# Kernel tuning notes

Hardware: AMD Instinct MI355X
Metric: run time of the kernel (lower is better)

## Reference

```python
import jax, jax.numpy as jnp
import numpy as np

# ClusterBlock passes CGAT(f0, f1, t, v, ...): CGAT's alpha positional gets v=325,
# so the LeakyReLU negative slope inside CGAT is 325.0 (faithful to source).
SLOPE = 325.0
NEG_INF = -9.0e15


def _leaky(x):
    return jnp.where(x >= 0, x, SLOPE * x)


def _cgat_stack(x, adj, W, Wb, Wt, a, offset):
    """Batched CGAT over (num_graph, k) sub-layers for one atrous offset.
    x: (b,v,t,f0); adj: (G,v,v) int; W:(G,K,f1,f0); Wb:(G,K,f1); Wt:(G,K,t); a:(G,K,2*f1).
    Returns (G,K,b,v,t,f1)."""
    b = x.shape[0]
    f1 = W.shape[-2]
    # h = leaky(W x + b): (G,K,b,v,t,f1)
    h = _leaky(jnp.einsum('bvtc,gkfc->gkbvtf', x, W) + Wb[:, :, None, None, None, :])
    # ht = mean over batch of Wt applied along t (no bias): (G,K,v,f1)
    ht = jnp.einsum('gkbvtf,gkt->gkvf', h, Wt) / b
    a1, a2 = a[..., :f1], a[..., f1:]          # attention vector halves
    ht_s = ht[:, :, offset::2]                  # sampled nodes (G,K,va,f1)
    # e[i,j] = leaky(a1.ht[sampled_j] + a2.ht[i]): (G,K,v,va)
    e = _leaky(jnp.einsum('gkjf,gkf->gkj', ht_s, a1)[:, :, None, :]
               + jnp.einsum('gkif,gkf->gki', ht, a2)[:, :, :, None])
    mask = (adj[:, None, :, offset::2] > 0)     # (G,1,v,va)
    att = jax.nn.softmax(jnp.where(mask, e, NEG_INF), axis=-1)
    # h_prime[b,i] = sum_j att[i,j] * h[b, sampled_j]
    hp = jnp.einsum('gkbjtf,gkij->gkbitf', h[:, :, :, offset::2], att)
    return _leaky(hp)


def setup_inputs() -> dict:
    key = jax.random.key(0)
    ks = jax.random.split(key, 8)
    B, V, T, F0, F1, K, G = 16, 325, 12, 64, 64, 4, 3
    x = jax.random.normal(ks[0], (B, V, T, F0), dtype=jnp.float32)
    graphs = jax.random.randint(ks[1], (G, V, V), 0, 2, dtype=jnp.int32)
    # params: axis 2 indexes the two atrous offsets (GC_layers1 / GC_layers2)
    W = jax.random.normal(ks[2], (G, K, 2, F1, F0), dtype=jnp.float32) * 0.02
    Wb = jax.random.normal(ks[3], (G, K, 2, F1), dtype=jnp.float32) * 0.02
    Wt = jax.random.normal(ks[4], (G, K, 2, T), dtype=jnp.float32) * 0.1
    a = jax.random.normal(ks[5], (G, K, 2, 2 * F1), dtype=jnp.float32) * 0.1
    cluster_W = jax.random.normal(ks[6], (G, K, T * F0), dtype=jnp.float32) * 0.02
    return {"x": x, "graphs": graphs, "W": W, "Wb": Wb, "Wt": Wt, "a": a,
            "cluster_W": cluster_W}


def reference(x, graphs, W, Wb, Wt, a, cluster_W):
    b, v, t, f0 = x.shape
    G = cluster_W.shape[0]
    xv = x.reshape(b, v, t * f0)
    # per-graph soft cluster assignments: (G,b,v,k)
    cluster = jax.nn.softmax(jnp.einsum('bvd,gkd->gbvk', xv, cluster_W), axis=-1)
    # gc1 (offset 0) + gc2 (offset 1): (G,K,b,v,t,f1)
    gc = (_cgat_stack(x, graphs, W[:, :, 0], Wb[:, :, 0], Wt[:, :, 0], a[:, :, 0], 0)
          + _cgat_stack(x, graphs, W[:, :, 1], Wb[:, :, 1], Wt[:, :, 1], a[:, :, 1], 1))
    # weight by cluster prob, sum over k, mean over graphs
    gc_act = jnp.einsum('gkbvtf,gbvk->bvtf', gc, cluster) / G
    return gc_act, cluster
```

## Files before the change

kernel.cpp:

```cpp
#include <hip/hip_runtime.h>
#include <math.h>

namespace {

typedef __attribute__((ext_vector_type(8))) short bf16x8;
typedef __attribute__((ext_vector_type(4))) float f32x4;

constexpr int B = 16, V = 325, T = 12, F = 64, K = 4, G = 3;
constexpr int D = T * F;
constexpr int ATT_R = 336;
constexpr int ATT_S = 192;
constexpr int OUT0 = B * V * T * F;
constexpr int HT_SZ = G * K * 2 * V * F;
constexpr float SLOPE_ = 325.0f;
constexpr float NEGINF = -9.0e15f;

__device__ __forceinline__ float leaky(float x) { return x >= 0.0f ? x : SLOPE_ * x; }

__device__ __forceinline__ unsigned short f2bf(float f) {
  unsigned int u = __float_as_uint(f);
  u = (u + 0x7fffu + ((u >> 16) & 1u)) >> 16;
  return (unsigned short)u;
}
__device__ __forceinline__ float bf2f(unsigned short h) {
  return __uint_as_float((unsigned int)h << 16);
}

__device__ __forceinline__ float wsum(float v) {
#pragma unroll
  for (int m = 32; m >= 1; m >>= 1) v += __shfl_xor(v, m);
  return v;
}
__device__ __forceinline__ float wmax(float v) {
#pragma unroll
  for (int m = 32; m >= 1; m >>= 1) v = fmaxf(v, __shfl_xor(v, m));
  return v;
}

__global__ __launch_bounds__(256) void k_cluster(const float* __restrict__ x,
                                                 const float* __restrict__ cw,
                                                 float* __restrict__ out) {
  const int bv = blockIdx.x;
  const int lane = threadIdx.x & 63, wave = threadIdx.x >> 6;
  __shared__ float lg[12];
  const float* xr = x + bv * D;
  for (int p = wave; p < 12; p += 4) {
    const float* wr = cw + p * D;
    float s = 0.f;
#pragma unroll
    for (int m = 0; m < 12; ++m) {
      const int d = lane + 64 * m;
      s = fmaf(xr[d], wr[d], s);
    }
    s = wsum(s);
    if (lane == 0) lg[p] = s;
  }
  __syncthreads();
  if (threadIdx.x < 3) {
    const int g = threadIdx.x;
    float m = lg[g * 4];
    for (int k = 1; k < 4; ++k) m = fmaxf(m, lg[g * 4 + k]);
    float e[4], s = 0.f;
    for (int k = 0; k < 4; ++k) { e[k] = expf(lg[g * 4 + k] - m); s += e[k]; }
    const float inv = 1.f / s;
    const int b = bv / V, v = bv % V;
    float* o = out + OUT0 + ((g * B + b) * V + v) * K;
    for (int k = 0; k < 4; ++k) o[k] = e[k] * inv;
  }
}

__global__ __launch_bounds__(512, 4) void k_ht(const float* __restrict__ x,
                                               const float* __restrict__ W,
                                               const float* __restrict__ Wbias,
                                               const float* __restrict__ Wt,
                                               float* __restrict__ ht) {
  const int v = blockIdx.x;
  const int tid = threadIdx.x;
  const int lane = tid & 63;
  const int wv = tid >> 6;
  const int lr = lane & 15, lg = lane >> 4;
  const int n = wv & 3, half = wv >> 2;

  __shared__ unsigned short Xhi[192 * 64];
  __shared__ unsigned short Xlo[192 * 64];
  __shared__ unsigned short Whi[64 * 64];
  __shared__ unsigned short Wlo[64 * 64];
  __shared__ float biasl[64];
  __shared__ float Wtl[12];
  __shared__ float red[4][2][16];

  for (int idx = tid; idx < 192 * 8; idx += 512) {
    const int row = idx >> 3, c0 = (idx & 7) * 8;
    const int bb = row / 12, tt = row % 12;
    const float* xp = x + ((bb * V + v) * T + tt) * F + c0;
    const float4 x0 = *(const float4*)xp;
    const float4 x1 = *(const float4*)(xp + 4);
    const float vals[8] = {x0.x, x0.y, x0.z, x0.w, x1.x, x1.y, x1.z, x1.w};
    union { unsigned short u[8]; uint4 q; } H, L;
#pragma unroll
    for (int e = 0; e < 8; ++e) {
      const unsigned short hh = f2bf(vals[e]);
      H.u[e] = hh;
      L.u[e] = f2bf(vals[e] - bf2f(hh));
    }
    const int off = (row * 128 + c0 * 2) ^ ((row & 7) << 4);
    *(uint4*)((char*)Xhi + off) = H.q;
    *(uint4*)((char*)Xlo + off) = L.q;
  }

  for (int gko = 0; gko < 24; ++gko) {
    {
      const int f = tid >> 3, c0 = (tid & 7) * 8;
      const float* wp = W + gko * (F * F) + f * 64 + c0;
      const float4 w0 = *(const float4*)wp;
      const float4 w1 = *(const float4*)(wp + 4);
      const float vals[8] = {w0.x, w0.y, w0.z, w0.w, w1.x, w1.y, w1.z, w1.w};
      union { unsigned short u[8]; uint4 q; } H, L;
#pragma unroll
      for (int e = 0; e < 8; ++e) {
        const unsigned short hh = f2bf(vals[e]);
        H.u[e] = hh;
        L.u[e] = f2bf(vals[e] - bf2f(hh));
      }
      const int off = (f * 128 + c0 * 2) ^ ((f & 7) << 4);
      *(uint4*)((char*)Whi + off) = H.q;
      *(uint4*)((char*)Wlo + off) = L.q;
      if (tid < 64) biasl[tid] = Wbias[gko * 64 + tid];
      else if (tid < 76) Wtl[tid - 64] = Wt[gko * 12 + (tid - 64)];
    }
    __syncthreads();

    float psum = 0.f;
    const float bv = biasl[n * 16 + lr];
    const int offB0 = ((n * 16 + lr) * 128) ^ (((n * 16 + lr) & 7) << 4);
#pragma unroll
    for (int i = 0; i < 6; ++i) {
      const int mt = half * 6 + i;
      const int arow = mt * 16 + lr;
      const int offA0 = (arow * 128) ^ ((arow & 7) << 4);
      f32x4 acc = (f32x4){0.f, 0.f, 0.f, 0.f};
#pragma unroll
      for (int kst = 0; kst < 2; ++kst) {
        const int kb = (kst * 32 + lg * 8) * 2;
        const bf16x8 ah = *(const bf16x8*)((const char*)Xhi + (offA0 ^ kb));
        const bf16x8 al = *(const bf16x8*)((const char*)Xlo + (offA0 ^ kb));
        const bf16x8 bh = *(const bf16x8*)((const char*)Whi + (offB0 ^ kb));
        const bf16x8 bl = *(const bf16x8*)((const char*)Wlo + (offB0 ^ kb));
        acc = __builtin_amdgcn_mfma_f32_16x16x32_bf16(ah, bh, acc, 0, 0, 0);
        acc = __builtin_amdgcn_mfma_f32_16x16x32_bf16(ah, bl, acc, 0, 0, 0);
        acc = __builtin_amdgcn_mfma_f32_16x16x32_bf16(al, bh, acc, 0, 0, 0);
      }
#pragma unroll
      for (int r = 0; r < 4; ++r) {
        const int row = mt * 16 + lg * 4 + r;
        psum = fmaf(leaky(acc[r] + bv), Wtl[row % 12], psum);
      }
    }
    psum += __shfl_xor(psum, 16);
    psum += __shfl_xor(psum, 32);
    if (lg == 0) red[n][half][lr] = psum;
    __syncthreads();
    if (tid < 64)
      ht[(gko * V + v) * 64 + tid] =
          (red[tid >> 4][0][tid & 15] + red[tid >> 4][1][tid & 15]) * (1.0f / 16.0f);
    __syncthreads();
  }
}

__global__ __launch_bounds__(256) void k_att(const float* __restrict__ ht,
                                             const float* __restrict__ a,
                                             const int* __restrict__ adj,
                                             unsigned short* __restrict__ att) {
  const int gko = blockIdx.x;
  const int o = gko & 1;
  const int g = gko >> 3;
  const int Vs = o ? 162 : 163;
  const int tid = threadIdx.x, lane = tid & 63, wave = tid >> 6;
  __shared__ float s1[163], s2[325];
  const float* htg = ht + gko * (V * F);
  const float* a1 = a + gko * 128;
  const float* a2 = a1 + 64;

  for (int d = wave; d < 325 + Vs; d += 4) {
    int row; const float* av;
    if (d < 325) { row = d;                 av = a2; }
    else         { row = o + 2 * (d - 325); av = a1; }
    float s = htg[row * 64 + lane] * av[lane];
    s = wsum(s);
    if (lane == 0) { if (d < 325) s2[d] = s; else s1[d - 325] = s; }
  }
  __syncthreads();

  const int* adjg = adj + g * (V * V);
  for (int i = wave; i < V; i += 4) {
    const float e0 = s2[i];
    float vj[3];
    float mx = NEGINF;
#pragma unroll
    for (int r = 0; r < 3; ++r) {
      const int j = lane + 64 * r;
      float val = NEGINF;
      if (j < Vs) {
        const float e = leaky(s1[j] + e0);
        const int ad = adjg[i * V + (o + 2 * j)];
        val = (ad > 0) ? e : NEGINF;
      }
      vj[r] = val;
      mx = fmaxf(mx, val);
    }
    mx = wmax(mx);
    float sum = 0.f, ex[3];
#pragma unroll
    for (int r = 0; r < 3; ++r) {
      const int j = lane + 64 * r;
      const float tt = (j < Vs) ? expf(vj[r] - mx) : 0.f;
      ex[r] = tt; sum += tt;
    }
    sum = wsum(sum);
    const float inv = 1.f / sum;
    unsigned short* ar = att + ((size_t)gko * ATT_R + i) * ATT_S;
#pragma unroll
    for (int r = 0; r < 3; ++r) {
      const int j = lane + 64 * r;
      ar[j] = (j < Vs) ? f2bf(ex[r] * inv) : 0;
    }
  }
  unsigned short* zb = att + ((size_t)gko * ATT_R + 325) * ATT_S;
  for (int idx = tid; idx < (ATT_R - V) * ATT_S; idx += 256) zb[idx] = 0;
}

__global__ __launch_bounds__(512, 2) void k_hp(const float* __restrict__ x,
                                               const float* __restrict__ W,
                                               const float* __restrict__ Wbias,
                                               const unsigned short* __restrict__ att,
                                               const float* __restrict__ cluster,
                                               float* __restrict__ out) {
  const int bid = blockIdx.x;
  const int o = bid & 1;
  const int g = (bid >> 1) % 3;
  const int bt = bid / 6;
  const int t = bt % 12;
  const int b = bt / 12;
  const int Vs = o ? 162 : 163;
  const int tid = threadIdx.x;
  const int lane = tid & 63;
  const int wv = tid >> 6;
  const int lr = lane & 15;
  const int lg = lane >> 4;

  __shared__ unsigned short Xl[176 * 64];
  __shared__ unsigned short Wlb[64 * 64];
  __shared__ unsigned short Htl[64 * 192];
  __shared__ float biasl[64];
  __shared__ float cll[336 * 4];

  for (int idx = tid; idx < 176 * 8; idx += 512) {
    const int j = idx >> 3, c0 = (idx & 7) * 8;
    union { unsigned short u[8]; uint4 q; } P;
    if (j < Vs) {
      const float* xp = x + ((b * V + (o + 2 * j)) * T + t) * F + c0;
      const float4 x0 = *(const float4*)xp;
      const float4 x1 = *(const float4*)(xp + 4);
      P.u[0] = f2bf(x0.x); P.u[1] = f2bf(x0.y); P.u[2] = f2bf(x0.z); P.u[3] = f2bf(x0.w);
      P.u[4] = f2bf(x1.x); P.u[5] = f2bf(x1.y); P.u[6] = f2bf(x1.z); P.u[7] = f2bf(x1.w);
    } else {
      P.q = make_uint4(0, 0, 0, 0);
    }
    *(uint4*)((char*)Xl + ((j * 128 + c0 * 2) ^ ((j & 7) << 4))) = P.q;
  }
  for (int i = tid; i < 336; i += 512) {
    float4 c4 = make_float4(0.f, 0.f, 0.f, 0.f);
    if (i < V) c4 = *(const float4*)(cluster + ((g * B + b) * V + i) * K);
    *(float4*)&cll[i * 4] = c4;
  }
  for (int idx = tid; idx < (64 * 192) / 8; idx += 512)
    ((uint4*)Htl)[idx] = make_uint4(0, 0, 0, 0);

  f32x4 accO[3][4];
#pragma unroll
  for (int s = 0; s < 3; ++s)
#pragma unroll
    for (int n = 0; n < 4; ++n) accO[s][n] = (f32x4){0.f, 0.f, 0.f, 0.f};

  for (int k = 0; k < K; ++k) {
    const int gko = (g * K + k) * 2 + o;
    __syncthreads();
    {
      const int f = tid >> 3, c0 = (tid & 7) * 8;
      const float* wp = W + gko * (F * F) + f * 64 + c0;
      const float4 w0 = *(const float4*)wp;
      const float4 w1 = *(const float4*)(wp + 4);
      union { unsigned short u[8]; uint4 q; } P;
      P.u[0] = f2bf(w0.x); P.u[1] = f2bf(w0.y); P.u[2] = f2bf(w0.z); P.u[3] = f2bf(w0.w);
      P.u[4] = f2bf(w1.x); P.u[5] = f2bf(w1.y); P.u[6] = f2bf(w1.z); P.u[7] = f2bf(w1.w);
      *(uint4*)((char*)Wlb + ((f * 128 + c0 * 2) ^ ((f & 7) << 4))) = P.q;
      if (tid < 64) biasl[tid] = Wbias[gko * 64 + tid];
    }
    __syncthreads();

    for (int s = 0; s < 6; ++s) {
      const int p = wv + 8 * s;
      if (p < 44) {
        const int mt = p >> 2, n = p & 3;
        f32x4 acc = (f32x4){0.f, 0.f, 0.f, 0.f};
#pragma unroll
        for (int kst = 0; kst < 2; ++kst) {
          const int j = mt * 16 + lr, k0 = kst * 32 + lg * 8;
          const bf16x8 af = *(const bf16x8*)((const char*)Xl + ((j * 128 + k0 * 2) ^ ((j & 7) << 4)));
          const int f = n * 16 + lr;
          const bf16x8 bf = *(const bf16x8*)((const char*)Wlb + ((f * 128 + k0 * 2) ^ ((f & 7) << 4)));
          acc = __builtin_amdgcn_mfma_f32_16x16x32_bf16(af, bf, acc, 0, 0, 0);
        }
        const int f = n * 16 + lr;
        const float bv = biasl[f];
        const int j0 = mt * 16 + lg * 4;
        union { unsigned short u[4]; uint2 q; } Pk;
#pragma unroll
        for (int r = 0; r < 4; ++r) {
          const float val = leaky(acc[r] + bv);
          Pk.u[r] = (j0 + r < Vs) ? f2bf(val) : 0;
        }
        *(uint2*)((char*)Htl + ((f * 384 + j0 * 2) ^ ((f & 7) << 4))) = Pk.q;
      }
    }
    __syncthreads();

    f32x4 accC[3][4];
#pragma unroll
    for (int s = 0; s < 3; ++s)
#pragma unroll
      for (int n = 0; n < 4; ++n) accC[s][n] = (f32x4){0.f, 0.f, 0.f, 0.f};

    const unsigned short* ab = att + (size_t)gko * (ATT_R * ATT_S);
#pragma unroll 2
    for (int kst = 0; kst < 6; ++kst) {
      const int kk0 = kst * 32 + lg * 8;
      bf16x8 bfr[4];
#pragma unroll
      for (int n = 0; n < 4; ++n) {
        const int f = n * 16 + lr;
        bfr[n] = *(const bf16x8*)((const char*)Htl + ((f * 384 + kk0 * 2) ^ ((f & 7) << 4)));
      }
#pragma unroll
      for (int s = 0; s < 3; ++s) {
        const int mt = wv + 8 * s;
        if (mt < 21) {
          const bf16x8 af = *(const bf16x8*)(ab + (mt * 16 + lr) * ATT_S + kk0);
#pragma unroll
          for (int n = 0; n < 4; ++n)
            accC[s][n] = __builtin_amdgcn_mfma_f32_16x16x32_bf16(af, bfr[n], accC[s][n], 0, 0, 0);
        }
      }
    }
#pragma unroll
    for (int s = 0; s < 3; ++s) {
      const int mt = wv + 8 * s;
      if (mt < 21) {
        const int i0 = mt * 16 + lg * 4;
#pragma unroll
        for (int r = 0; r < 4; ++r) {
          const float clv = cll[(i0 + r) * 4 + k];
#pragma unroll
          for (int n = 0; n < 4; ++n)
            accO[s][n][r] += leaky(accC[s][n][r]) * clv;
        }
      }
    }
  }

#pragma unroll
  for (int s = 0; s < 3; ++s) {
    const int mt = wv + 8 * s;
    if (mt < 21) {
      const int i0 = mt * 16 + lg * 4;
#pragma unroll
      for (int r = 0; r < 4; ++r) {
        const int i = i0 + r;
        if (i < V) {
          float* op = out + ((b * V + i) * T + t) * F + lr;
#pragma unroll
          for (int n = 0; n < 4; ++n)
            atomicAdd(op + n * 16, accO[s][n][r] * (1.0f / 3.0f));
        }
      }
    }
  }
}

}

extern "C" void kernel_launch(void* const* d_in, const int* in_sizes, int n_in,
                              void* d_out, int out_size, void* d_ws, size_t ws_size,
                              hipStream_t stream) {
  const float* x   = (const float*)d_in[0];
  const int*   adj = (const int*)d_in[1];
  const float* W   = (const float*)d_in[2];
  const float* Wb  = (const float*)d_in[3];
  const float* Wt  = (const float*)d_in[4];
  const float* a   = (const float*)d_in[5];
  const float* cw  = (const float*)d_in[6];
  float* out = (float*)d_out;
  float* ws  = (float*)d_ws;

  float* ht = ws;
  unsigned short* attw = (unsigned short*)(ws + HT_SZ);

  hipMemsetAsync(out, 0, (size_t)OUT0 * sizeof(float), stream);
  k_cluster<<<B * V, 256, 0, stream>>>(x, cw, out);
  k_ht<<<V, 512, 0, stream>>>(x, W, Wb, Wt, ht);
  k_att<<<G * K * 2, 256, 0, stream>>>(ht, a, adj, attw);
  k_hp<<<B * T * G * 2, 512, 0, stream>>>(x, W, Wb, attw, out + OUT0, out);
}
```

Measured before the change: 397.3 us.

## Replace output atomics with partial buffers plus reduction kernel; keep W fragments in registers

k_hp now writes each (graph, offset) block's weighted result to a separate partial buffer in workspace, and a new k_red kernel sums the six partials and scales by 1/3. This replaces the float atomicAdd epilogue and the output memset, provided the workspace is large enough; otherwise it falls back to the atomic path. W fragments and bias are loaded straight into registers and prefetched for the next k, which removes the shared W tile and one barrier per k. It also zeroes only the padding part of Htl, raises launch bounds to 4 blocks per SM, and fully unrolls the attention loop. The cost is roughly 100MB of extra partial-buffer traffic and higher register pressure.

```diff
diff --git a/kernel.cpp b/kernel.cpp
--- a/kernel.cpp
+++ b/kernel.cpp
@@ -14,6 +14,12 @@
 constexpr int HT_SZ = G * K * 2 * V * F;
 constexpr float SLOPE_ = 325.0f;
 constexpr float NEGINF = -9.0e15f;
+
+constexpr size_t HT_BYTES   = (size_t)HT_SZ * 4;
+constexpr size_t ATT_BYTES  = (size_t)24 * ATT_R * ATT_S * 2;
+constexpr size_t PART_OFF_B = HT_BYTES + ATT_BYTES;
+constexpr size_t PART_BYTES = (size_t)6 * 192 * 336 * 64 * 4;
+constexpr size_t WS_NEED    = PART_OFF_B + PART_BYTES;
 
 __device__ __forceinline__ float leaky(float x) { return x >= 0.0f ? x : SLOPE_ * x; }
 
@@ -229,12 +235,13 @@
   for (int idx = tid; idx < (ATT_R - V) * ATT_S; idx += 256) zb[idx] = 0;
 }
 
-__global__ __launch_bounds__(512, 2) void k_hp(const float* __restrict__ x,
+__global__ __launch_bounds__(512, 4) void k_hp(const float* __restrict__ x,
                                                const float* __restrict__ W,
                                                const float* __restrict__ Wbias,
                                                const unsigned short* __restrict__ att,
                                                const float* __restrict__ cluster,
-                                               float* __restrict__ out) {
+                                               float* __restrict__ out,
+                                               float* __restrict__ part) {
   const int bid = blockIdx.x;
   const int o = bid & 1;
   const int g = (bid >> 1) % 3;
@@ -247,11 +254,11 @@
   const int wv = tid >> 6;
   const int lr = lane & 15;
   const int lg = lane >> 4;
+  const int n = wv & 3;
+  const int halfw = wv >> 2;
 
   __shared__ unsigned short Xl[176 * 64];
-  __shared__ unsigned short Wlb[64 * 64];
   __shared__ unsigned short Htl[64 * 192];
-  __shared__ float biasl[64];
   __shared__ float cll[336 * 4];
 
   for (int idx = tid; idx < 176 * 8; idx += 512) {
@@ -273,55 +280,78 @@
     if (i < V) c4 = *(const float4*)(cluster + ((g * B + b) * V + i) * K);
     *(float4*)&cll[i * 4] = c4;
   }
-  for (int idx = tid; idx < (64 * 192) / 8; idx += 512)
-    ((uint4*)Htl)[idx] = make_uint4(0, 0, 0, 0);
+  if (tid < 128) {
+    const int f = tid >> 1, j0 = 176 + (tid & 1) * 8;
+    *(uint4*)((char*)Htl + ((f * 384 + j0 * 2) ^ ((f & 7) << 4))) = make_uint4(0, 0, 0, 0);
+  }
+
+  const int f_row = n * 16 + lr;
+  float4 praw[2][2];
+  float bias_now;
+  {
+    const int gko0 = (g * K + 0) * 2 + o;
+    const float* wp = W + gko0 * (F * F) + f_row * 64 + lg * 8;
+#pragma unroll
+    for (int kst = 0; kst < 2; ++kst) {
+      praw[kst][0] = *(const float4*)(wp + kst * 32);
+      praw[kst][1] = *(const float4*)(wp + kst * 32 + 4);
+    }
+    bias_now = Wbias[gko0 * 64 + f_row];
+  }
 
   f32x4 accO[3][4];
 #pragma unroll
   for (int s = 0; s < 3; ++s)
 #pragma unroll
-    for (int n = 0; n < 4; ++n) accO[s][n] = (f32x4){0.f, 0.f, 0.f, 0.f};
+    for (int nn = 0; nn < 4; ++nn) accO[s][nn] = (f32x4){0.f, 0.f, 0.f, 0.f};
 
   for (int k = 0; k < K; ++k) {
     const int gko = (g * K + k) * 2 + o;
     __syncthreads();
-    {
-      const int f = tid >> 3, c0 = (tid & 7) * 8;
-      const float* wp = W + gko * (F * F) + f * 64 + c0;
-      const float4 w0 = *(const float4*)wp;
-      const float4 w1 = *(const float4*)(wp + 4);
-      union { unsigned short u[8]; uint4 q; } P;
-      P.u[0] = f2bf(w0.x); P.u[1] = f2bf(w0.y); P.u[2] = f2bf(w0.z); P.u[3] = f2bf(w0.w);
-      P.u[4] = f2bf(w1.x); P.u[5] = f2bf(w1.y); P.u[6] = f2bf(w1.z); P.u[7] = f2bf(w1.w);
-      *(uint4*)((char*)Wlb + ((f * 128 + c0 * 2) ^ ((f & 7) << 4))) = P.q;
-      if (tid < 64) biasl[tid] = Wbias[gko * 64 + tid];
-    }
-    __syncthreads();
-
+
+    bf16x8 wf[2];
+#pragma unroll
+    for (int kst = 0; kst < 2; ++kst) {
+      const float vals[8] = {praw[kst][0].x, praw[kst][0].y, praw[kst][0].z, praw[kst][0].w,
+                             praw[kst][1].x, praw[kst][1].y, praw[kst][1].z, praw[kst][1].w};
+      union { unsigned short u[8]; bf16x8 v; } P;
+#pragma unroll
+      for (int e = 0; e < 8; ++e) P.u[e] = f2bf(vals[e]);
+      wf[kst] = P.v;
+    }
+    const float bnow = bias_now;
+
+#pragma unroll
     for (int s = 0; s < 6; ++s) {
-      const int p = wv + 8 * s;
-      if (p < 44) {
-        const int mt = p >> 2, n = p & 3;
+      const int mt = halfw + 2 * s;
+      if (mt < 11) {
         f32x4 acc = (f32x4){0.f, 0.f, 0.f, 0.f};
 #pragma unroll
         for (int kst = 0; kst < 2; ++kst) {
           const int j = mt * 16 + lr, k0 = kst * 32 + lg * 8;
           const bf16x8 af = *(const bf16x8*)((const char*)Xl + ((j * 128 + k0 * 2) ^ ((j & 7) << 4)));
-          const int f = n * 16 + lr;
-          const bf16x8 bf = *(const bf16x8*)((const char*)Wlb + ((f * 128 + k0 * 2) ^ ((f & 7) << 4)));
-          acc = __builtin_amdgcn_mfma_f32_16x16x32_bf16(af, bf, acc, 0, 0, 0);
-        }
-        const int f = n * 16 + lr;
-        const float bv = biasl[f];
+          acc = __builtin_amdgcn_mfma_f32_16x16x32_bf16(af, wf[kst], acc, 0, 0, 0);
+        }
         const int j0 = mt * 16 + lg * 4;
         union { unsigned short u[4]; uint2 q; } Pk;
 #pragma unroll
         for (int r = 0; r < 4; ++r) {
-          const float val = leaky(acc[r] + bv);
+          const float val = leaky(acc[r] + bnow);
           Pk.u[r] = (j0 + r < Vs) ? f2bf(val) : 0;
         }
-        *(uint2*)((char*)Htl + ((f * 384 + j0 * 2) ^ ((f & 7) << 4))) = Pk.q;
-      }
+        *(uint2*)((char*)Htl + ((f_row * 384 + j0 * 2) ^ ((f_row & 7) << 4))) = Pk.q;
+      }
+    }
+
+    if (k < 3) {
+      const int gkon = (g * K + (k + 1)) * 2 + o;
+      const float* wp = W + gkon * (F * F) + f_row * 64 + lg * 8;
+#pragma unroll
+      for (int kst = 0; kst < 2; ++kst) {
+        praw[kst][0] = *(const float4*)(wp + kst * 32);
+        praw[kst][1] = *(const float4*)(wp + kst * 32 + 4);
+      }
+      bias_now = Wbias[gkon * 64 + f_row];
     }
     __syncthreads();
 
@@ -329,17 +359,17 @@
 #pragma unroll
     for (int s = 0; s < 3; ++s)
 #pragma unroll
-      for (int n = 0; n < 4; ++n) accC[s][n] = (f32x4){0.f, 0.f, 0.f, 0.f};
+      for (int nn = 0; nn < 4; ++nn) accC[s][nn] = (f32x4){0.f, 0.f, 0.f, 0.f};
 
     const unsigned short* ab = att + (size_t)gko * (ATT_R * ATT_S);
-#pragma unroll 2
+#pragma unroll
     for (int kst = 0; kst < 6; ++kst) {
       const int kk0 = kst * 32 + lg * 8;
       bf16x8 bfr[4];
 #pragma unroll
-      for (int n = 0; n < 4; ++n) {
-        const int f = n * 16 + lr;
-        bfr[n] = *(const bf16x8*)((const char*)Htl + ((f * 384 + kk0 * 2) ^ ((f & 7) << 4)));
+      for (int nn = 0; nn < 4; ++nn) {
+        const int f = nn * 16 + lr;
+        bfr[nn] = *(const bf16x8*)((const char*)Htl + ((f * 384 + kk0 * 2) ^ ((f & 7) << 4)));
       }
 #pragma unroll
       for (int s = 0; s < 3; ++s) {
@@ -347,8 +377,8 @@
         if (mt < 21) {
           const bf16x8 af = *(const bf16x8*)(ab + (mt * 16 + lr) * ATT_S + kk0);
 #pragma unroll
-          for (int n = 0; n < 4; ++n)
-            accC[s][n] = __builtin_amdgcn_mfma_f32_16x16x32_bf16(af, bfr[n], accC[s][n], 0, 0, 0);
+          for (int nn = 0; nn < 4; ++nn)
+            accC[s][nn] = __builtin_amdgcn_mfma_f32_16x16x32_bf16(af, bfr[nn], accC[s][nn], 0, 0, 0);
         }
       }
     }
@@ -361,30 +391,69 @@
         for (int r = 0; r < 4; ++r) {
           const float clv = cll[(i0 + r) * 4 + k];
 #pragma unroll
-          for (int n = 0; n < 4; ++n)
-            accO[s][n][r] += leaky(accC[s][n][r]) * clv;
-        }
-      }
-    }
-  }
-
-#pragma unroll
-  for (int s = 0; s < 3; ++s) {
-    const int mt = wv + 8 * s;
-    if (mt < 21) {
-      const int i0 = mt * 16 + lg * 4;
-#pragma unroll
-      for (int r = 0; r < 4; ++r) {
-        const int i = i0 + r;
-        if (i < V) {
-          float* op = out + ((b * V + i) * T + t) * F + lr;
-#pragma unroll
-          for (int n = 0; n < 4; ++n)
-            atomicAdd(op + n * 16, accO[s][n][r] * (1.0f / 3.0f));
-        }
-      }
-    }
-  }
+          for (int nn = 0; nn < 4; ++nn)
+            accO[s][nn][r] += leaky(accC[s][nn][r]) * clv;
+        }
+      }
+    }
+  }
+
+  if (part) {
+    float* pb = part + (((size_t)(g * 2 + o) * 192 + bt) * 336) * 64;
+#pragma unroll
+    for (int s = 0; s < 3; ++s) {
+      const int mt = wv + 8 * s;
+      if (mt < 21) {
+        const int i0 = mt * 16 + lg * 4;
+#pragma unroll
+        for (int r = 0; r < 4; ++r) {
+          float* op = pb + (i0 + r) * 64 + lr;
+#pragma unroll
+          for (int nn = 0; nn < 4; ++nn) op[nn * 16] = accO[s][nn][r];
+        }
+      }
+    }
+  } else {
+#pragma unroll
+    for (int s = 0; s < 3; ++s) {
+      const int mt = wv + 8 * s;
+      if (mt < 21) {
+        const int i0 = mt * 16 + lg * 4;
+#pragma unroll
+        for (int r = 0; r < 4; ++r) {
+          const int i = i0 + r;
+          if (i < V) {
+            float* op = out + ((b * V + i) * T + t) * F + lr;
+#pragma unroll
+            for (int nn = 0; nn < 4; ++nn)
+              atomicAdd(op + nn * 16, accO[s][nn][r] * (1.0f / 3.0f));
+          }
+        }
+      }
+    }
+  }
+}
+
+__global__ __launch_bounds__(256) void k_red(const float* __restrict__ part,
+                                             float* __restrict__ out) {
+  const int idx = blockIdx.x * 256 + threadIdx.x;
+  const int f4 = idx & 15;
+  const int r = idx >> 4;
+  const int t = r % T;
+  const int r2 = r / T;
+  const int v = r2 % V;
+  const int b = r2 / V;
+  const size_t base = (((size_t)(b * T + t)) * 336 + v) * 16 + f4;
+  f32x4 s = (f32x4){0.f, 0.f, 0.f, 0.f};
+#pragma unroll
+  for (int p = 0; p < 6; ++p) {
+    const float4 q = *(const float4*)(part + (base + (size_t)p * 192 * 336 * 16) * 4);
+    s[0] += q.x; s[1] += q.y; s[2] += q.z; s[3] += q.w;
+  }
+  float4 o4;
+  o4.x = s[0] * (1.0f / 3.0f); o4.y = s[1] * (1.0f / 3.0f);
+  o4.z = s[2] * (1.0f / 3.0f); o4.w = s[3] * (1.0f / 3.0f);
+  *(float4*)(out + (size_t)idx * 4) = o4;
 }
 
 }
@@ -400,14 +469,16 @@
   const float* a   = (const float*)d_in[5];
   const float* cw  = (const float*)d_in[6];
   float* out = (float*)d_out;
-  float* ws  = (float*)d_ws;
-
-  float* ht = ws;
-  unsigned short* attw = (unsigned short*)(ws + HT_SZ);
-
-  hipMemsetAsync(out, 0, (size_t)OUT0 * sizeof(float), stream);
+  char*  ws  = (char*)d_ws;
+
+  float* ht = (float*)ws;
+  unsigned short* attw = (unsigned short*)(ws + HT_BYTES);
+  float* part = (ws_size >= WS_NEED) ? (float*)(ws + PART_OFF_B) : nullptr;
+
+  if (!part) hipMemsetAsync(out, 0, (size_t)OUT0 * sizeof(float), stream);
   k_cluster<<<B * V, 256, 0, stream>>>(x, cw, out);
   k_ht<<<V, 512, 0, stream>>>(x, W, Wb, Wt, ht);
   k_att<<<G * K * 2, 256, 0, stream>>>(ht, a, adj, attw);
-  k_hp<<<B * T * G * 2, 512, 0, stream>>>(x, W, Wb, attw, out + OUT0, out);
-}
+  k_hp<<<B * T * G * 2, 512, 0, stream>>>(x, W, Wb, attw, out + OUT0, out, part);
+  if (part) k_red<<<OUT0 / 4 / 256, 256, 0, stream>>>(part, out);
+}
```

After: 499.7 us. 1.26x slower.
